# Kernel optimization log

Hardware: AMD Instinct MI355X
Metric: run time of the kernel (lower is better)

The kernel has to match this reference:

```python
import jax, jax.numpy as jnp
import numpy as np

D_MODEL = 1024
D_FF = 4 * D_MODEL
NUM_EXPERTS = 8
TOP_K = 2
BATCH, SEQ = 2, 2048


def setup_inputs() -> dict:
    key = jax.random.key(0)
    ks = jax.random.split(key, 6)
    s_in = 1.0 / np.sqrt(D_MODEL)
    s_ff = 1.0 / np.sqrt(D_FF)
    x = jax.random.normal(ks[0], (BATCH, SEQ, D_MODEL), dtype=jnp.float32)
    Wg = jax.random.uniform(ks[1], (D_MODEL, NUM_EXPERTS), minval=-s_in, maxval=s_in, dtype=jnp.float32)
    W1 = jax.random.uniform(ks[2], (NUM_EXPERTS, D_MODEL, D_FF), minval=-s_in, maxval=s_in, dtype=jnp.float32)
    b1 = jax.random.uniform(ks[3], (NUM_EXPERTS, D_FF), minval=-s_in, maxval=s_in, dtype=jnp.float32)
    W2 = jax.random.uniform(ks[4], (NUM_EXPERTS, D_FF, D_MODEL), minval=-s_ff, maxval=s_ff, dtype=jnp.float32)
    b2 = jax.random.uniform(ks[5], (NUM_EXPERTS, D_MODEL), minval=-s_ff, maxval=s_ff, dtype=jnp.float32)
    return {"x": x, "Wg": Wg, "W1": W1, "b1": b1, "W2": W2, "b2": b2}


def reference(x, Wg, W1, b1, W2, b2):
    B, S, D = x.shape
    x_flat = x.reshape(-1, D)                      # [T, D]
    gate_logits = x_flat @ Wg                      # [T, E] (eval mode: no noise)
    gate_probs = jax.nn.softmax(gate_logits, axis=-1)
    top_v, top_i = jax.lax.top_k(gate_probs, TOP_K)            # [T, k]
    top_v = top_v / (jnp.sum(top_v, axis=-1, keepdims=True) + 1e-8)
    out = jnp.zeros_like(x_flat)
    for e in range(NUM_EXPERTS):
        # combine weight for expert e: sum of normalized top-k probs routed here
        w_e = jnp.sum(jnp.where(top_i == e, top_v, 0.0), axis=-1)   # [T]
        h = jax.nn.gelu(x_flat @ W1[e] + b1[e], approximate=False)  # [T, F]
        y = h @ W2[e] + b2[e]                                       # [T, D]
        out = out + w_e[:, None] * y
    return out.reshape(B, S, D)
```

## Files before the change

### kernel.cpp

```cpp
#include <hip/hip_runtime.h>
#include <math.h>

typedef __attribute__((ext_vector_type(8))) short short8;
typedef __attribute__((ext_vector_type(4))) float f32x4;
typedef unsigned short u16;

#define NT 4096
#define DM 1024
#define DF 4096
#define NE 8
#define HROWS 9216
#define TIT 72
#define YROWS (2 * NT + 8)

static __device__ __forceinline__ u16 f2bf(float f) {
  union { float f; unsigned u; } v; v.f = f;
  return (u16)((v.u + 0x7fffu + ((v.u >> 16) & 1u)) >> 16);
}

static __device__ __forceinline__ float fast_gelu(float x) {
  float x2 = x * x;
  float z = x * __builtin_fmaf(x2, 0.1029392294f, 2.302118131f);
  float e, r;
  asm("v_exp_f32 %0, %1" : "=v"(e) : "v"(z));
  float e1 = e + 1.0f;
  asm("v_rcp_f32 %0, %1" : "=v"(r) : "v"(e1));
  return __builtin_fmaf(-x, r, x);
}

static __device__ __forceinline__ void gload16(const void* g, void* l) {
  __builtin_amdgcn_global_load_lds((const __attribute__((address_space(1))) void*)g,
                                   (__attribute__((address_space(3))) void*)l, 16, 0, 0);
}

static __device__ __forceinline__ int xcd_swz(int bid, int nwg) {
  int per = nwg >> 3;
  return (bid & 7) * per + (bid >> 3);
}

__global__ __launch_bounds__(256) void gate_k(const float* __restrict__ x,
                                              const float* __restrict__ Wg,
                                              int* __restrict__ te,
                                              float* __restrict__ tw,
                                              u16* __restrict__ xbf) {
  int t = blockIdx.x * 4 + (threadIdx.x >> 6);
  int l = threadIdx.x & 63;
  float a0=0,a1=0,a2=0,a3=0,a4=0,a5=0,a6=0,a7=0;
  const float* xr = x + (size_t)t * DM;
  for (int k = l; k < DM; k += 64) {
    float xv = xr[k];
    const float4* wp = (const float4*)(Wg + k * 8);
    float4 w0 = wp[0], w1 = wp[1];
    a0 += xv * w0.x; a1 += xv * w0.y; a2 += xv * w0.z; a3 += xv * w0.w;
    a4 += xv * w1.x; a5 += xv * w1.y; a6 += xv * w1.z; a7 += xv * w1.w;
  }
  u16* xo = xbf + (size_t)t * DM;
#pragma unroll
  for (int h = 0; h < 2; ++h) {
    int k = h * 512 + l * 8;
    float4 a = *(const float4*)(xr + k);
    float4 b = *(const float4*)(xr + k + 4);
    short8 o8 = { (short)f2bf(a.x), (short)f2bf(a.y), (short)f2bf(a.z), (short)f2bf(a.w),
                  (short)f2bf(b.x), (short)f2bf(b.y), (short)f2bf(b.z), (short)f2bf(b.w) };
    *(short8*)(xo + k) = o8;
  }
#pragma unroll
  for (int s = 32; s >= 1; s >>= 1) {
    a0 += __shfl_down(a0, s); a1 += __shfl_down(a1, s);
    a2 += __shfl_down(a2, s); a3 += __shfl_down(a3, s);
    a4 += __shfl_down(a4, s); a5 += __shfl_down(a5, s);
    a6 += __shfl_down(a6, s); a7 += __shfl_down(a7, s);
  }
  if (l == 0) {
    float lg[8] = {a0,a1,a2,a3,a4,a5,a6,a7};
    float m = lg[0];
#pragma unroll
    for (int e = 1; e < 8; ++e) m = fmaxf(m, lg[e]);
    float p[8], s = 0.f;
#pragma unroll
    for (int e = 0; e < 8; ++e) { p[e] = expf(lg[e] - m); s += p[e]; }
#pragma unroll
    for (int e = 0; e < 8; ++e) p[e] /= s;
    int i0 = 0; float v0 = p[0];
#pragma unroll
    for (int e = 1; e < 8; ++e) if (p[e] > v0) { v0 = p[e]; i0 = e; }
    int i1 = -1; float v1 = -1.f;
#pragma unroll
    for (int e = 0; e < 8; ++e) {
      if (e == i0) continue;
      if (p[e] > v1) { v1 = p[e]; i1 = e; }
    }
    float norm = v0 + v1 + 1e-8f;
    te[t*2]   = i0; te[t*2+1] = i1;
    tw[t*2]   = v0 / norm; tw[t*2+1] = v1 / norm;
  }
}

__global__ __launch_bounds__(256) void route_k(const int* __restrict__ te,
                                               const float* __restrict__ tw,
                                               int* __restrict__ meta,
                                               int* __restrict__ lt,
                                               float* __restrict__ lw) {
  int i = blockIdx.x * 256 + threadIdx.x;
  if (i >= NT * 2) return;
  int e = te[i];
  float w = tw[i];
  int pos = atomicAdd(&meta[e], 1);
  lt[e * NT + pos] = i;
  lw[e * NT + pos] = w;
}

__global__ __launch_bounds__(256) void finalize_k(int* __restrict__ meta,
                                                  int* __restrict__ lt,
                                                  float* __restrict__ lw) {
  __shared__ int s_cnt[8], s_pc[8];
  if (threadIdx.x == 0) {
    int base = 0, nt_ = 0;
    for (int e = 0; e < 8; ++e) {
      int c = meta[e];
      int pc = (c + 127) & ~127;
      s_cnt[e] = c; s_pc[e] = pc;
      meta[8 + e] = pc;
      meta[16 + e] = base;
      base += pc;
      for (int mt = 0; mt < pc / 128; ++mt) meta[32 + nt_++] = (e << 16) | mt;
    }
    meta[24] = nt_;
  }
  __syncthreads();
  for (int e = 0; e < 8; ++e) {
    int c = s_cnt[e], pc = s_pc[e];
    for (int i = c + (int)threadIdx.x; i < pc; i += 256) {
      lt[e * NT + i] = 2 * NT;
      lw[e * NT + i] = 0.f;
    }
  }
}

__global__ __launch_bounds__(256) void prep_wT(const float* __restrict__ in,
                                               u16* __restrict__ out, int K, int N) {
  const int e = blockIdx.z;
  const int n0 = blockIdx.x * 64, k0 = blockIdx.y * 64;
  const float* ie = in + (size_t)e * K * N;
  u16* oe = out + (size_t)e * K * N;
  __shared__ u16 t[64 * 72];
  const int tid = threadIdx.x;
  const int kr = tid >> 4, nq = (tid & 15) * 4;
#pragma unroll
  for (int it = 0; it < 4; ++it) {
    int k = it * 16 + kr;
    float4 v = *(const float4*)(ie + (size_t)(k0 + k) * N + n0 + nq);
    t[(nq + 0) * 72 + k] = f2bf(v.x);
    t[(nq + 1) * 72 + k] = f2bf(v.y);
    t[(nq + 2) * 72 + k] = f2bf(v.z);
    t[(nq + 3) * 72 + k] = f2bf(v.w);
  }
  __syncthreads();
#pragma unroll
  for (int it = 0; it < 2; ++it) {
    int idx = it * 256 + tid;
    int n = idx >> 3, kc = idx & 7;
    short8 v = *(const short8*)&t[n * 72 + kc * 8];
    *(short8*)(oe + (size_t)(n0 + n) * K + k0 + kc * 8) = v;
  }
}

#define STAGE4(b)                                            \
  do {                                                       \
    gload16(pa0, laA + (b) * 4096 + lda0);                   \
    gload16(pa1, laA + (b) * 4096 + lda1);                   \
    gload16(pb0, laB + (b) * 4096 + lda0);                   \
    gload16(pb1, laB + (b) * 4096 + lda1);                   \
    pa0 += 32; pa1 += 32; pb0 += 32; pb1 += 32;              \
  } while (0)

__global__ __launch_bounds__(256) void ffn1_k(const u16* __restrict__ xbf,
                                              const u16* __restrict__ W1T,
                                              const float* __restrict__ b1,
                                              const int* __restrict__ lt,
                                              const int* __restrict__ meta,
                                              u16* __restrict__ H) {
  const int vid = xcd_swz(blockIdx.x, (DF / 128) * TIT);
  const int nt = vid & 31;
  const int ti = vid >> 5;
  if (ti >= meta[24]) return;
  const int em = meta[32 + ti];
  const int e = em >> 16, mt = em & 0xffff;
  const int rbase = meta[16 + e];

  __shared__ u16 As[2 * 4096];
  __shared__ u16 Bs[2 * 4096];

  const int tid = threadIdx.x, lane = tid & 63, wv = tid >> 6;
  const int wm = wv >> 1, wn = wv & 1, l15 = lane & 15, l4 = lane >> 4;

  int r0i = tid >> 2, s0 = tid & 3;
  int r1i = (256 + tid) >> 2;
  int kg0 = s0 ^ ((r0i >> 1) & 3);
  int kg1 = s0 ^ ((r1i >> 1) & 3);
  int tok0 = lt[e * NT + mt * 128 + r0i] >> 1; if (tok0 >= NT) tok0 = 0;
  int tok1 = lt[e * NT + mt * 128 + r1i] >> 1; if (tok1 >= NT) tok1 = 0;
  const u16* pa0 = xbf + (size_t)tok0 * DM + kg0 * 8;
  const u16* pa1 = xbf + (size_t)tok1 * DM + kg1 * 8;
  const u16* pb0 = W1T + ((size_t)e * DF + nt * 128 + r0i) * DM + kg0 * 8;
  const u16* pb1 = W1T + ((size_t)e * DF + nt * 128 + r1i) * DM + kg1 * 8;
  u16* laA = As; u16* laB = Bs;
  const int lda0 = (wv * 64) * 8, lda1 = (256 + wv * 64) * 8;

  int aoff[4], boff[4];
#pragma unroll
  for (int i = 0; i < 4; ++i) {
    int ra = wm * 64 + i * 16 + l15;
    aoff[i] = ra * 32 + (l4 ^ ((ra >> 1) & 3)) * 8;
    int rb = wn * 64 + i * 16 + l15;
    boff[i] = rb * 32 + (l4 ^ ((rb >> 1) & 3)) * 8;
  }

  f32x4 acc[4][4];
#pragma unroll
  for (int mi = 0; mi < 4; ++mi)
#pragma unroll
    for (int ni = 0; ni < 4; ++ni) acc[mi][ni] = 0.f;

  STAGE4(0);
  asm volatile("s_waitcnt vmcnt(0)" ::: "memory");
  __builtin_amdgcn_s_barrier();

  const int NK = DM / 32;
  int cur = 0;
  for (int ks = 0; ks < NK; ++ks) {
    if (ks + 1 < NK) STAGE4(cur ^ 1);
    short8 af[4], bf_[4];
#pragma unroll
    for (int i = 0; i < 4; ++i) {
      af[i]  = *(const short8*)&As[cur * 4096 + aoff[i]];
      bf_[i] = *(const short8*)&Bs[cur * 4096 + boff[i]];
    }
#pragma unroll
    for (int mi = 0; mi < 4; ++mi)
#pragma unroll
      for (int ni = 0; ni < 4; ++ni)
        acc[mi][ni] = __builtin_amdgcn_mfma_f32_16x16x32_bf16(af[mi], bf_[ni], acc[mi][ni], 0, 0, 0);
    asm volatile("s_waitcnt vmcnt(0)" ::: "memory");
    __builtin_amdgcn_s_barrier();
    cur ^= 1;
  }

  const size_t hrow0 = (size_t)rbase + mt * 128;
#pragma unroll
  for (int mi = 0; mi < 4; ++mi) {
#pragma unroll
    for (int ni = 0; ni < 4; ++ni) {
      int gn = nt * 128 + wn * 64 + ni * 16 + l15;
      float bias = b1[e * DF + gn];
      int rr = wm * 64 + mi * 16 + l4 * 4;
#pragma unroll
      for (int j = 0; j < 4; ++j) {
        float v = fast_gelu(acc[mi][ni][j] + bias);
        H[(hrow0 + rr + j) * DF + gn] = f2bf(v);
      }
    }
  }
}

template <bool USEY>
__global__ __launch_bounds__(256) void ffn2_k(const u16* __restrict__ H,
                                              const u16* __restrict__ W2T,
                                              const float* __restrict__ b2,
                                              const int* __restrict__ lt,
                                              const float* __restrict__ lw,
                                              const int* __restrict__ meta,
                                              float* __restrict__ Y,
                                              float* __restrict__ out) {
  const int vid = xcd_swz(blockIdx.x, (DM / 128) * TIT);
  const int nt = vid & 7;
  const int ti = vid >> 3;
  if (ti >= meta[24]) return;
  const int em = meta[32 + ti];
  const int e = em >> 16, mt = em & 0xffff;
  const int rbase = meta[16 + e];

  __shared__ u16 As[2 * 4096];
  __shared__ u16 Bs[2 * 4096];
  __shared__ int s_ts[128];
  __shared__ float s_w[128];

  const int tid = threadIdx.x, lane = tid & 63, wv = tid >> 6;
  const int wm = wv >> 1, wn = wv & 1, l15 = lane & 15, l4 = lane >> 4;

  if (tid < 128) {
    s_ts[tid] = lt[e * NT + mt * 128 + tid];
    s_w[tid]  = lw[e * NT + mt * 128 + tid];
  }

  int r0i = tid >> 2, s0 = tid & 3;
  int r1i = (256 + tid) >> 2;
  int kg0 = s0 ^ ((r0i >> 1) & 3);
  int kg1 = s0 ^ ((r1i >> 1) & 3);
  const u16* pa0 = H + ((size_t)rbase + mt * 128 + r0i) * DF + kg0 * 8;
  const u16* pa1 = H + ((size_t)rbase + mt * 128 + r1i) * DF + kg1 * 8;
  const u16* pb0 = W2T + ((size_t)e * DM + nt * 128 + r0i) * DF + kg0 * 8;
  const u16* pb1 = W2T + ((size_t)e * DM + nt * 128 + r1i) * DF + kg1 * 8;
  u16* laA = As; u16* laB = Bs;
  const int lda0 = (wv * 64) * 8, lda1 = (256 + wv * 64) * 8;

  int aoff[4], boff[4];
#pragma unroll
  for (int i = 0; i < 4; ++i) {
    int ra = wm * 64 + i * 16 + l15;
    aoff[i] = ra * 32 + (l4 ^ ((ra >> 1) & 3)) * 8;
    int rb = wn * 64 + i * 16 + l15;
    boff[i] = rb * 32 + (l4 ^ ((rb >> 1) & 3)) * 8;
  }

  f32x4 acc[4][4];
#pragma unroll
  for (int mi = 0; mi < 4; ++mi)
#pragma unroll
    for (int ni = 0; ni < 4; ++ni) acc[mi][ni] = 0.f;

  STAGE4(0);
  asm volatile("s_waitcnt vmcnt(0)" ::: "memory");
  __builtin_amdgcn_s_barrier();

  const int NK = DF / 32;
  int cur = 0;
  for (int ks = 0; ks < NK; ++ks) {
    if (ks + 1 < NK) STAGE4(cur ^ 1);
    short8 af[4], bf_[4];
#pragma unroll
    for (int i = 0; i < 4; ++i) {
      af[i]  = *(const short8*)&As[cur * 4096 + aoff[i]];
      bf_[i] = *(const short8*)&Bs[cur * 4096 + boff[i]];
    }
#pragma unroll
    for (int mi = 0; mi < 4; ++mi)
#pragma unroll
      for (int ni = 0; ni < 4; ++ni)
        acc[mi][ni] = __builtin_amdgcn_mfma_f32_16x16x32_bf16(af[mi], bf_[ni], acc[mi][ni], 0, 0, 0);
    asm volatile("s_waitcnt vmcnt(0)" ::: "memory");
    __builtin_amdgcn_s_barrier();
    cur ^= 1;
  }

#pragma unroll
  for (int mi = 0; mi < 4; ++mi) {
#pragma unroll
    for (int ni = 0; ni < 4; ++ni) {
      int gn = nt * 128 + wn * 64 + ni * 16 + l15;
      float bias = b2[e * DM + gn];
      int rr = wm * 64 + mi * 16 + l4 * 4;
#pragma unroll
      for (int j = 0; j < 4; ++j) {
        int r = rr + j;
        float w = s_w[r];
        int ts = s_ts[r];
        float v = w * (acc[mi][ni][j] + bias);
        if (USEY) {
          Y[(size_t)ts * DM + gn] = v;
        } else {
          int tok = ts >> 1;
          if (tok >= NT) tok = 0;
          atomicAdd(out + (size_t)tok * DM + gn, v);
        }
      }
    }
  }
}

__global__ __launch_bounds__(256) void combine_k(const float* __restrict__ Y,
                                                 float* __restrict__ out) {
  size_t i4 = (size_t)blockIdx.x * 256 + threadIdx.x;
  size_t t = i4 >> 8;
  int c4 = (int)(i4 & 255) * 4;
  const float4 a = *(const float4*)(Y + (2 * t) * DM + c4);
  const float4 b = *(const float4*)(Y + (2 * t + 1) * DM + c4);
  float4 o = { a.x + b.x, a.y + b.y, a.z + b.z, a.w + b.w };
  *(float4*)(out + t * DM + c4) = o;
}

extern "C" void kernel_launch(void* const* d_in, const int* in_sizes, int n_in,
                              void* d_out, int out_size, void* d_ws, size_t ws_size,
                              hipStream_t stream) {
  const float* x  = (const float*)d_in[0];
  const float* Wg = (const float*)d_in[1];
  const float* W1 = (const float*)d_in[2];
  const float* b1 = (const float*)d_in[3];
  const float* W2 = (const float*)d_in[4];
  const float* b2 = (const float*)d_in[5];
  float* out = (float*)d_out;

  char* ws = (char*)d_ws;
  size_t o = 0;
  auto take = [&](size_t sz) { size_t p = o; o = (o + sz + 1023) & ~(size_t)1023; return p; };

  int*   meta = (int*)(ws + take(1024));
  int*   te   = (int*)(ws + take((size_t)NT * 2 * 4));
  float* tw   = (float*)(ws + take((size_t)NT * 2 * 4));
  int*   lt   = (int*)(ws + take((size_t)NE * NT * 4));
  float* lw   = (float*)(ws + take((size_t)NE * NT * 4));
  u16*   xbf  = (u16*)(ws + take((size_t)NT * DM * 2));
  u16*   W1T  = (u16*)(ws + take((size_t)NE * DM * DF * 2));
  u16*   H    = (u16*)(ws + take((size_t)HROWS * DF * 2));
  size_t needB = o;
  size_t ySz = (size_t)YROWS * DM * 4;
  size_t needA = needB + ((size_t)NE * DM * DF * 2 + 1024) + (ySz + 1024);

  bool pathA = (ws_size >= needA);
  u16*   W2T;
  float* Y = nullptr;
  if (pathA) {
    W2T = (u16*)(ws + take((size_t)NE * DM * DF * 2));
    Y   = (float*)(ws + take(ySz));
  } else {
    W2T = W1T;
  }

  hipMemsetAsync(meta, 0, 1024, stream);
  if (!pathA) hipMemsetAsync(out, 0, (size_t)NT * DM * 4, stream);

  gate_k<<<NT / 4, 256, 0, stream>>>(x, Wg, te, tw, xbf);
  route_k<<<(NT * 2) / 256, 256, 0, stream>>>(te, tw, meta, lt, lw);
  finalize_k<<<1, 256, 0, stream>>>(meta, lt, lw);
  prep_wT<<<dim3(DF / 64, DM / 64, NE), 256, 0, stream>>>(W1, W1T, DM, DF);
  if (pathA)
    prep_wT<<<dim3(DM / 64, DF / 64, NE), 256, 0, stream>>>(W2, W2T, DF, DM);

  ffn1_k<<<(DF / 128) * TIT, 256, 0, stream>>>(xbf, W1T, b1, lt, meta, H);

  if (!pathA)
    prep_wT<<<dim3(DM / 64, DF / 64, NE), 256, 0, stream>>>(W2, W2T, DF, DM);

  if (pathA) {
    ffn2_k<true><<<(DM / 128) * TIT, 256, 0, stream>>>(H, W2T, b2, lt, lw, meta, Y, out);
    combine_k<<<NT, 256, 0, stream>>>(Y, out);
  } else {
    ffn2_k<false><<<(DM / 128) * TIT, 256, 0, stream>>>(H, W2T, b2, lt, lw, meta, Y, out);
  }
}
```

Before: 406.1 us.

## Use BK=64 single-buffered tiles and split-K the second FFN GEMM

Both expert GEMM kernels now load a 64-wide K tile into a single LDS buffer with an 8-way XOR swizzle. They use two barriers per step instead of double-buffered 32-wide tiles, which halves the loop iterations but no longer overlaps loads with MFMA. When the workspace is large enough, ffn2 is split along K into two halves writing separate Y buffers, and combine_k sums them. This doubles the block count for the low-parallelism second GEMM, at the cost of extra Y traffic and workspace.

```diff
diff --git a/kernel.cpp b/kernel.cpp
--- a/kernel.cpp
+++ b/kernel.cpp
@@ -12,6 +12,7 @@
 #define HROWS 9216
 #define TIT 72
 #define YROWS (2 * NT + 8)
+#define BK 64
 
 static __device__ __forceinline__ u16 f2bf(float f) {
   union { float f; unsigned u; } v; v.f = f;
@@ -165,15 +166,6 @@
   }
 }
 
-#define STAGE4(b)                                            \
-  do {                                                       \
-    gload16(pa0, laA + (b) * 4096 + lda0);                   \
-    gload16(pa1, laA + (b) * 4096 + lda1);                   \
-    gload16(pb0, laB + (b) * 4096 + lda0);                   \
-    gload16(pb1, laB + (b) * 4096 + lda1);                   \
-    pa0 += 32; pa1 += 32; pb0 += 32; pb1 += 32;              \
-  } while (0)
-
 __global__ __launch_bounds__(256) void ffn1_k(const u16* __restrict__ xbf,
                                               const u16* __restrict__ W1T,
                                               const float* __restrict__ b1,
@@ -188,32 +180,32 @@
   const int e = em >> 16, mt = em & 0xffff;
   const int rbase = meta[16 + e];
 
-  __shared__ u16 As[2 * 4096];
-  __shared__ u16 Bs[2 * 4096];
+  __shared__ u16 As[128 * BK];
+  __shared__ u16 Bs[128 * BK];
 
   const int tid = threadIdx.x, lane = tid & 63, wv = tid >> 6;
   const int wm = wv >> 1, wn = wv & 1, l15 = lane & 15, l4 = lane >> 4;
 
-  int r0i = tid >> 2, s0 = tid & 3;
-  int r1i = (256 + tid) >> 2;
-  int kg0 = s0 ^ ((r0i >> 1) & 3);
-  int kg1 = s0 ^ ((r1i >> 1) & 3);
-  int tok0 = lt[e * NT + mt * 128 + r0i] >> 1; if (tok0 >= NT) tok0 = 0;
-  int tok1 = lt[e * NT + mt * 128 + r1i] >> 1; if (tok1 >= NT) tok1 = 0;
-  const u16* pa0 = xbf + (size_t)tok0 * DM + kg0 * 8;
-  const u16* pa1 = xbf + (size_t)tok1 * DM + kg1 * 8;
-  const u16* pb0 = W1T + ((size_t)e * DF + nt * 128 + r0i) * DM + kg0 * 8;
-  const u16* pb1 = W1T + ((size_t)e * DF + nt * 128 + r1i) * DM + kg1 * 8;
-  u16* laA = As; u16* laB = Bs;
-  const int lda0 = (wv * 64) * 8, lda1 = (256 + wv * 64) * 8;
+  const int c8 = tid & 7, r0 = tid >> 3;
+  const int cs = c8 ^ (r0 & 7);
+  const u16* pa[4]; const u16* pb[4];
+#pragma unroll
+  for (int it = 0; it < 4; ++it) {
+    int r = r0 + it * 32;
+    int tok = lt[e * NT + mt * 128 + r] >> 1; if (tok >= NT) tok = 0;
+    pa[it] = xbf + (size_t)tok * DM + cs * 8;
+    pb[it] = W1T + ((size_t)e * DF + nt * 128 + r) * DM + cs * 8;
+  }
+  u16* ldsA = As + (size_t)wv * 64 * 8;
+  u16* ldsB = Bs + (size_t)wv * 64 * 8;
 
   int aoff[4], boff[4];
 #pragma unroll
   for (int i = 0; i < 4; ++i) {
     int ra = wm * 64 + i * 16 + l15;
-    aoff[i] = ra * 32 + (l4 ^ ((ra >> 1) & 3)) * 8;
+    aoff[i] = ra * BK + (l4 ^ (ra & 7)) * 8;
     int rb = wn * 64 + i * 16 + l15;
-    boff[i] = rb * 32 + (l4 ^ ((rb >> 1) & 3)) * 8;
+    boff[i] = rb * BK + (l4 ^ (rb & 7)) * 8;
   }
 
   f32x4 acc[4][4];
@@ -222,28 +214,32 @@
 #pragma unroll
     for (int ni = 0; ni < 4; ++ni) acc[mi][ni] = 0.f;
 
-  STAGE4(0);
-  asm volatile("s_waitcnt vmcnt(0)" ::: "memory");
-  __builtin_amdgcn_s_barrier();
-
-  const int NK = DM / 32;
-  int cur = 0;
+  const int NK = DM / BK;
   for (int ks = 0; ks < NK; ++ks) {
-    if (ks + 1 < NK) STAGE4(cur ^ 1);
-    short8 af[4], bf_[4];
-#pragma unroll
-    for (int i = 0; i < 4; ++i) {
-      af[i]  = *(const short8*)&As[cur * 4096 + aoff[i]];
-      bf_[i] = *(const short8*)&Bs[cur * 4096 + boff[i]];
-    }
-#pragma unroll
-    for (int mi = 0; mi < 4; ++mi)
-#pragma unroll
-      for (int ni = 0; ni < 4; ++ni)
-        acc[mi][ni] = __builtin_amdgcn_mfma_f32_16x16x32_bf16(af[mi], bf_[ni], acc[mi][ni], 0, 0, 0);
-    asm volatile("s_waitcnt vmcnt(0)" ::: "memory");
-    __builtin_amdgcn_s_barrier();
-    cur ^= 1;
+    __syncthreads();
+#pragma unroll
+    for (int it = 0; it < 4; ++it) {
+      gload16(pa[it], ldsA + it * 2048);
+      gload16(pb[it], ldsB + it * 2048);
+      pa[it] += BK; pb[it] += BK;
+    }
+    __syncthreads();
+
+    short8 af[2][4], bf_[2][4];
+#pragma unroll
+    for (int h = 0; h < 2; ++h)
+#pragma unroll
+      for (int i = 0; i < 4; ++i) {
+        af[h][i]  = *(const short8*)&As[aoff[i] ^ (h * 32)];
+        bf_[h][i] = *(const short8*)&Bs[boff[i] ^ (h * 32)];
+      }
+#pragma unroll
+    for (int h = 0; h < 2; ++h)
+#pragma unroll
+      for (int mi = 0; mi < 4; ++mi)
+#pragma unroll
+        for (int ni = 0; ni < 4; ++ni)
+          acc[mi][ni] = __builtin_amdgcn_mfma_f32_16x16x32_bf16(af[h][mi], bf_[h][ni], acc[mi][ni], 0, 0, 0);
   }
 
   const size_t hrow0 = (size_t)rbase + mt * 128;
@@ -263,7 +259,7 @@
   }
 }
 
-template <bool USEY>
+template <bool USEY, int NZ>
 __global__ __launch_bounds__(256) void ffn2_k(const u16* __restrict__ H,
                                               const u16* __restrict__ W2T,
                                               const float* __restrict__ b2,
@@ -272,16 +268,18 @@
                                               const int* __restrict__ meta,
                                               float* __restrict__ Y,
                                               float* __restrict__ out) {
-  const int vid = xcd_swz(blockIdx.x, (DM / 128) * TIT);
+  const int vid = xcd_swz(blockIdx.x, (DM / 128) * TIT * NZ);
   const int nt = vid & 7;
-  const int ti = vid >> 3;
+  const int kz = (NZ == 2) ? ((vid >> 3) & 1) : 0;
+  const int ti = (NZ == 2) ? (vid >> 4) : (vid >> 3);
   if (ti >= meta[24]) return;
   const int em = meta[32 + ti];
   const int e = em >> 16, mt = em & 0xffff;
   const int rbase = meta[16 + e];
-
-  __shared__ u16 As[2 * 4096];
-  __shared__ u16 Bs[2 * 4096];
+  const int KOFF = kz * (DF / NZ);
+
+  __shared__ u16 As[128 * BK];
+  __shared__ u16 Bs[128 * BK];
   __shared__ int s_ts[128];
   __shared__ float s_w[128];
 
@@ -293,24 +291,25 @@
     s_w[tid]  = lw[e * NT + mt * 128 + tid];
   }
 
-  int r0i = tid >> 2, s0 = tid & 3;
-  int r1i = (256 + tid) >> 2;
-  int kg0 = s0 ^ ((r0i >> 1) & 3);
-  int kg1 = s0 ^ ((r1i >> 1) & 3);
-  const u16* pa0 = H + ((size_t)rbase + mt * 128 + r0i) * DF + kg0 * 8;
-  const u16* pa1 = H + ((size_t)rbase + mt * 128 + r1i) * DF + kg1 * 8;
-  const u16* pb0 = W2T + ((size_t)e * DM + nt * 128 + r0i) * DF + kg0 * 8;
-  const u16* pb1 = W2T + ((size_t)e * DM + nt * 128 + r1i) * DF + kg1 * 8;
-  u16* laA = As; u16* laB = Bs;
-  const int lda0 = (wv * 64) * 8, lda1 = (256 + wv * 64) * 8;
+  const int c8 = tid & 7, r0 = tid >> 3;
+  const int cs = c8 ^ (r0 & 7);
+  const u16* pa[4]; const u16* pb[4];
+#pragma unroll
+  for (int it = 0; it < 4; ++it) {
+    int r = r0 + it * 32;
+    pa[it] = H + ((size_t)rbase + mt * 128 + r) * DF + KOFF + cs * 8;
+    pb[it] = W2T + ((size_t)e * DM + nt * 128 + r) * DF + KOFF + cs * 8;
+  }
+  u16* ldsA = As + (size_t)wv * 64 * 8;
+  u16* ldsB = Bs + (size_t)wv * 64 * 8;
 
   int aoff[4], boff[4];
 #pragma unroll
   for (int i = 0; i < 4; ++i) {
     int ra = wm * 64 + i * 16 + l15;
-    aoff[i] = ra * 32 + (l4 ^ ((ra >> 1) & 3)) * 8;
+    aoff[i] = ra * BK + (l4 ^ (ra & 7)) * 8;
     int rb = wn * 64 + i * 16 + l15;
-    boff[i] = rb * 32 + (l4 ^ ((rb >> 1) & 3)) * 8;
+    boff[i] = rb * BK + (l4 ^ (rb & 7)) * 8;
   }
 
   f32x4 acc[4][4];
@@ -319,28 +318,32 @@
 #pragma unroll
     for (int ni = 0; ni < 4; ++ni) acc[mi][ni] = 0.f;
 
-  STAGE4(0);
-  asm volatile("s_waitcnt vmcnt(0)" ::: "memory");
-  __builtin_amdgcn_s_barrier();
-
-  const int NK = DF / 32;
-  int cur = 0;
+  const int NK = (DF / NZ) / BK;
   for (int ks = 0; ks < NK; ++ks) {
-    if (ks + 1 < NK) STAGE4(cur ^ 1);
-    short8 af[4], bf_[4];
-#pragma unroll
-    for (int i = 0; i < 4; ++i) {
-      af[i]  = *(const short8*)&As[cur * 4096 + aoff[i]];
-      bf_[i] = *(const short8*)&Bs[cur * 4096 + boff[i]];
-    }
-#pragma unroll
-    for (int mi = 0; mi < 4; ++mi)
-#pragma unroll
-      for (int ni = 0; ni < 4; ++ni)
-        acc[mi][ni] = __builtin_amdgcn_mfma_f32_16x16x32_bf16(af[mi], bf_[ni], acc[mi][ni], 0, 0, 0);
-    asm volatile("s_waitcnt vmcnt(0)" ::: "memory");
-    __builtin_amdgcn_s_barrier();
-    cur ^= 1;
+    __syncthreads();
+#pragma unroll
+    for (int it = 0; it < 4; ++it) {
+      gload16(pa[it], ldsA + it * 2048);
+      gload16(pb[it], ldsB + it * 2048);
+      pa[it] += BK; pb[it] += BK;
+    }
+    __syncthreads();
+
+    short8 af[2][4], bf_[2][4];
+#pragma unroll
+    for (int h = 0; h < 2; ++h)
+#pragma unroll
+      for (int i = 0; i < 4; ++i) {
+        af[h][i]  = *(const short8*)&As[aoff[i] ^ (h * 32)];
+        bf_[h][i] = *(const short8*)&Bs[boff[i] ^ (h * 32)];
+      }
+#pragma unroll
+    for (int h = 0; h < 2; ++h)
+#pragma unroll
+      for (int mi = 0; mi < 4; ++mi)
+#pragma unroll
+        for (int ni = 0; ni < 4; ++ni)
+          acc[mi][ni] = __builtin_amdgcn_mfma_f32_16x16x32_bf16(af[h][mi], bf_[h][ni], acc[mi][ni], 0, 0, 0);
   }
 
 #pragma unroll
@@ -348,7 +351,7 @@
 #pragma unroll
     for (int ni = 0; ni < 4; ++ni) {
       int gn = nt * 128 + wn * 64 + ni * 16 + l15;
-      float bias = b2[e * DM + gn];
+      float bias = (kz == 0) ? b2[e * DM + gn] : 0.f;
       int rr = wm * 64 + mi * 16 + l4 * 4;
 #pragma unroll
       for (int j = 0; j < 4; ++j) {
@@ -357,7 +360,7 @@
         int ts = s_ts[r];
         float v = w * (acc[mi][ni][j] + bias);
         if (USEY) {
-          Y[(size_t)ts * DM + gn] = v;
+          Y[((size_t)kz * YROWS + ts) * DM + gn] = v;
         } else {
           int tok = ts >> 1;
           if (tok >= NT) tok = 0;
@@ -369,13 +372,18 @@
 }
 
 __global__ __launch_bounds__(256) void combine_k(const float* __restrict__ Y,
-                                                 float* __restrict__ out) {
+                                                 float* __restrict__ out, int nz) {
   size_t i4 = (size_t)blockIdx.x * 256 + threadIdx.x;
   size_t t = i4 >> 8;
   int c4 = (int)(i4 & 255) * 4;
   const float4 a = *(const float4*)(Y + (2 * t) * DM + c4);
   const float4 b = *(const float4*)(Y + (2 * t + 1) * DM + c4);
   float4 o = { a.x + b.x, a.y + b.y, a.z + b.z, a.w + b.w };
+  if (nz == 2) {
+    const float4 c = *(const float4*)(Y + ((size_t)YROWS + 2 * t) * DM + c4);
+    const float4 d = *(const float4*)(Y + ((size_t)YROWS + 2 * t + 1) * DM + c4);
+    o.x += c.x + d.x; o.y += c.y + d.y; o.z += c.z + d.z; o.w += c.w + d.w;
+  }
   *(float4*)(out + t * DM + c4) = o;
 }
 
@@ -404,37 +412,41 @@
   u16*   H    = (u16*)(ws + take((size_t)HROWS * DF * 2));
   size_t needB = o;
   size_t ySz = (size_t)YROWS * DM * 4;
-  size_t needA = needB + ((size_t)NE * DM * DF * 2 + 1024) + (ySz + 1024);
-
-  bool pathA = (ws_size >= needA);
+  size_t needA  = needB + ((size_t)NE * DM * DF * 2 + 1024) + (ySz + 1024);
+  size_t needA2 = needA + ySz + 1024;
+
+  int nz = (ws_size >= needA2) ? 2 : (ws_size >= needA ? 1 : 0);
   u16*   W2T;
   float* Y = nullptr;
-  if (pathA) {
+  if (nz > 0) {
     W2T = (u16*)(ws + take((size_t)NE * DM * DF * 2));
-    Y   = (float*)(ws + take(ySz));
+    Y   = (float*)(ws + take((size_t)nz * ySz));
   } else {
     W2T = W1T;
   }
 
   hipMemsetAsync(meta, 0, 1024, stream);
-  if (!pathA) hipMemsetAsync(out, 0, (size_t)NT * DM * 4, stream);
+  if (nz == 0) hipMemsetAsync(out, 0, (size_t)NT * DM * 4, stream);
 
   gate_k<<<NT / 4, 256, 0, stream>>>(x, Wg, te, tw, xbf);
   route_k<<<(NT * 2) / 256, 256, 0, stream>>>(te, tw, meta, lt, lw);
   finalize_k<<<1, 256, 0, stream>>>(meta, lt, lw);
   prep_wT<<<dim3(DF / 64, DM / 64, NE), 256, 0, stream>>>(W1, W1T, DM, DF);
-  if (pathA)
+  if (nz > 0)
     prep_wT<<<dim3(DM / 64, DF / 64, NE), 256, 0, stream>>>(W2, W2T, DF, DM);
 
   ffn1_k<<<(DF / 128) * TIT, 256, 0, stream>>>(xbf, W1T, b1, lt, meta, H);
 
-  if (!pathA)
+  if (nz == 0)
     prep_wT<<<dim3(DM / 64, DF / 64, NE), 256, 0, stream>>>(W2, W2T, DF, DM);
 
-  if (pathA) {
-    ffn2_k<true><<<(DM / 128) * TIT, 256, 0, stream>>>(H, W2T, b2, lt, lw, meta, Y, out);
-    combine_k<<<NT, 256, 0, stream>>>(Y, out);
+  if (nz == 2) {
+    ffn2_k<true, 2><<<(DM / 128) * TIT * 2, 256, 0, stream>>>(H, W2T, b2, lt, lw, meta, Y, out);
+    combine_k<<<NT, 256, 0, stream>>>(Y, out, 2);
+  } else if (nz == 1) {
+    ffn2_k<true, 1><<<(DM / 128) * TIT, 256, 0, stream>>>(H, W2T, b2, lt, lw, meta, Y, out);
+    combine_k<<<NT, 256, 0, stream>>>(Y, out, 1);
   } else {
-    ffn2_k<false><<<(DM / 128) * TIT, 256, 0, stream>>>(H, W2T, b2, lt, lw, meta, Y, out);
-  }
-}
+    ffn2_k<false, 1><<<(DM / 128) * TIT, 256, 0, stream>>>(H, W2T, b2, lt, lw, meta, Y, out);
+  }
+}
```

After: 417.5 us. +2.8%, slower.

## Replace double-buffered LDS staging with a single buffer in both FFN GEMMs

Applied to the files above, without the earlier changes.

Both expert GEMM kernels (ffn1 and ffn2) now stage each K-slice into one LDS buffer instead of two ping-pong buffers. Each iteration is bracketed by two __syncthreads, one before and one after the loads. This halves the LDS footprint per block, which could allow more resident blocks per CU. In exchange, the global-to-LDS load of the next slice no longer overlaps the MFMA work on the current slice, so every K step pays the full load latency plus an extra barrier.

```diff
diff --git a/kernel.cpp b/kernel.cpp
--- a/kernel.cpp
+++ b/kernel.cpp
@@ -165,15 +165,6 @@
   }
 }
 
-#define STAGE4(b)                                            \
-  do {                                                       \
-    gload16(pa0, laA + (b) * 4096 + lda0);                   \
-    gload16(pa1, laA + (b) * 4096 + lda1);                   \
-    gload16(pb0, laB + (b) * 4096 + lda0);                   \
-    gload16(pb1, laB + (b) * 4096 + lda1);                   \
-    pa0 += 32; pa1 += 32; pb0 += 32; pb1 += 32;              \
-  } while (0)
-
 __global__ __launch_bounds__(256) void ffn1_k(const u16* __restrict__ xbf,
                                               const u16* __restrict__ W1T,
                                               const float* __restrict__ b1,
@@ -188,8 +179,8 @@
   const int e = em >> 16, mt = em & 0xffff;
   const int rbase = meta[16 + e];
 
-  __shared__ u16 As[2 * 4096];
-  __shared__ u16 Bs[2 * 4096];
+  __shared__ u16 As[128 * 32];
+  __shared__ u16 Bs[128 * 32];
 
   const int tid = threadIdx.x, lane = tid & 63, wv = tid >> 6;
   const int wm = wv >> 1, wn = wv & 1, l15 = lane & 15, l4 = lane >> 4;
@@ -204,7 +195,6 @@
   const u16* pa1 = xbf + (size_t)tok1 * DM + kg1 * 8;
   const u16* pb0 = W1T + ((size_t)e * DF + nt * 128 + r0i) * DM + kg0 * 8;
   const u16* pb1 = W1T + ((size_t)e * DF + nt * 128 + r1i) * DM + kg1 * 8;
-  u16* laA = As; u16* laB = Bs;
   const int lda0 = (wv * 64) * 8, lda1 = (256 + wv * 64) * 8;
 
   int aoff[4], boff[4];
@@ -222,28 +212,25 @@
 #pragma unroll
     for (int ni = 0; ni < 4; ++ni) acc[mi][ni] = 0.f;
 
-  STAGE4(0);
-  asm volatile("s_waitcnt vmcnt(0)" ::: "memory");
-  __builtin_amdgcn_s_barrier();
-
   const int NK = DM / 32;
-  int cur = 0;
   for (int ks = 0; ks < NK; ++ks) {
-    if (ks + 1 < NK) STAGE4(cur ^ 1);
+    __syncthreads();
+    gload16(pa0, As + lda0); gload16(pa1, As + lda1);
+    gload16(pb0, Bs + lda0); gload16(pb1, Bs + lda1);
+    pa0 += 32; pa1 += 32; pb0 += 32; pb1 += 32;
+    __syncthreads();
+
     short8 af[4], bf_[4];
 #pragma unroll
     for (int i = 0; i < 4; ++i) {
-      af[i]  = *(const short8*)&As[cur * 4096 + aoff[i]];
-      bf_[i] = *(const short8*)&Bs[cur * 4096 + boff[i]];
+      af[i]  = *(const short8*)&As[aoff[i]];
+      bf_[i] = *(const short8*)&Bs[boff[i]];
     }
 #pragma unroll
     for (int mi = 0; mi < 4; ++mi)
 #pragma unroll
       for (int ni = 0; ni < 4; ++ni)
         acc[mi][ni] = __builtin_amdgcn_mfma_f32_16x16x32_bf16(af[mi], bf_[ni], acc[mi][ni], 0, 0, 0);
-    asm volatile("s_waitcnt vmcnt(0)" ::: "memory");
-    __builtin_amdgcn_s_barrier();
-    cur ^= 1;
   }
 
   const size_t hrow0 = (size_t)rbase + mt * 128;
@@ -280,8 +267,8 @@
   const int e = em >> 16, mt = em & 0xffff;
   const int rbase = meta[16 + e];
 
-  __shared__ u16 As[2 * 4096];
-  __shared__ u16 Bs[2 * 4096];
+  __shared__ u16 As[128 * 32];
+  __shared__ u16 Bs[128 * 32];
   __shared__ int s_ts[128];
   __shared__ float s_w[128];
 
@@ -301,7 +288,6 @@
   const u16* pa1 = H + ((size_t)rbase + mt * 128 + r1i) * DF + kg1 * 8;
   const u16* pb0 = W2T + ((size_t)e * DM + nt * 128 + r0i) * DF + kg0 * 8;
   const u16* pb1 = W2T + ((size_t)e * DM + nt * 128 + r1i) * DF + kg1 * 8;
-  u16* laA = As; u16* laB = Bs;
   const int lda0 = (wv * 64) * 8, lda1 = (256 + wv * 64) * 8;
 
   int aoff[4], boff[4];
@@ -319,28 +305,25 @@
 #pragma unroll
     for (int ni = 0; ni < 4; ++ni) acc[mi][ni] = 0.f;
 
-  STAGE4(0);
-  asm volatile("s_waitcnt vmcnt(0)" ::: "memory");
-  __builtin_amdgcn_s_barrier();
-
   const int NK = DF / 32;
-  int cur = 0;
   for (int ks = 0; ks < NK; ++ks) {
-    if (ks + 1 < NK) STAGE4(cur ^ 1);
+    __syncthreads();
+    gload16(pa0, As + lda0); gload16(pa1, As + lda1);
+    gload16(pb0, Bs + lda0); gload16(pb1, Bs + lda1);
+    pa0 += 32; pa1 += 32; pb0 += 32; pb1 += 32;
+    __syncthreads();
+
     short8 af[4], bf_[4];
 #pragma unroll
     for (int i = 0; i < 4; ++i) {
-      af[i]  = *(const short8*)&As[cur * 4096 + aoff[i]];
-      bf_[i] = *(const short8*)&Bs[cur * 4096 + boff[i]];
+      af[i]  = *(const short8*)&As[aoff[i]];
+      bf_[i] = *(const short8*)&Bs[boff[i]];
     }
 #pragma unroll
     for (int mi = 0; mi < 4; ++mi)
 #pragma unroll
       for (int ni = 0; ni < 4; ++ni)
         acc[mi][ni] = __builtin_amdgcn_mfma_f32_16x16x32_bf16(af[mi], bf_[ni], acc[mi][ni], 0, 0, 0);
-    asm volatile("s_waitcnt vmcnt(0)" ::: "memory");
-    __builtin_amdgcn_s_barrier();
-    cur ^= 1;
   }
 
 #pragma unroll
```

Measured after the change: 354.0 us. 12.8% less time.

## Deepen global-to-LDS prefetch so two stages are in flight in both FFN GEMMs

Applied to the files above, without the earlier changes.

The K-loops of both expert GEMMs now issue loads for stages 0 and 1 up front. Each iteration waits with vmcnt(4), so only the current stage has to have landed while the next stays in flight. The freed buffer is refilled after the compute and an LDS-read barrier. This aims to hide more global-load latency than the old scheme, which waited for all loads at the end of each step. It adds one more barrier per iteration and relies on exact vmcnt counting with the two LDS buffers.

```diff
diff --git a/kernel.cpp b/kernel.cpp
--- a/kernel.cpp
+++ b/kernel.cpp
@@ -165,13 +165,13 @@
   }
 }
 
-#define STAGE4(b)                                            \
-  do {                                                       \
-    gload16(pa0, laA + (b) * 4096 + lda0);                   \
-    gload16(pa1, laA + (b) * 4096 + lda1);                   \
-    gload16(pb0, laB + (b) * 4096 + lda0);                   \
-    gload16(pb1, laB + (b) * 4096 + lda1);                   \
-    pa0 += 32; pa1 += 32; pb0 += 32; pb1 += 32;              \
+#define STAGE(b)                                                   \
+  do {                                                             \
+    gload16(pa0, As + (b) * 4096 + lda0);                          \
+    gload16(pa1, As + (b) * 4096 + lda1);                          \
+    gload16(pb0, Bs + (b) * 4096 + lda0);                          \
+    gload16(pb1, Bs + (b) * 4096 + lda1);                          \
+    pa0 += 32; pa1 += 32; pb0 += 32; pb1 += 32;                    \
   } while (0)
 
 __global__ __launch_bounds__(256) void ffn1_k(const u16* __restrict__ xbf,
@@ -204,7 +204,6 @@
   const u16* pa1 = xbf + (size_t)tok1 * DM + kg1 * 8;
   const u16* pb0 = W1T + ((size_t)e * DF + nt * 128 + r0i) * DM + kg0 * 8;
   const u16* pb1 = W1T + ((size_t)e * DF + nt * 128 + r1i) * DM + kg1 * 8;
-  u16* laA = As; u16* laB = Bs;
   const int lda0 = (wv * 64) * 8, lda1 = (256 + wv * 64) * 8;
 
   int aoff[4], boff[4];
@@ -222,14 +221,15 @@
 #pragma unroll
     for (int ni = 0; ni < 4; ++ni) acc[mi][ni] = 0.f;
 
-  STAGE4(0);
-  asm volatile("s_waitcnt vmcnt(0)" ::: "memory");
-  __builtin_amdgcn_s_barrier();
-
   const int NK = DM / 32;
+  STAGE(0);
+  STAGE(1);
   int cur = 0;
   for (int ks = 0; ks < NK; ++ks) {
-    if (ks + 1 < NK) STAGE4(cur ^ 1);
+    if (ks + 1 < NK) asm volatile("s_waitcnt vmcnt(4)" ::: "memory");
+    else             asm volatile("s_waitcnt vmcnt(0)" ::: "memory");
+    __builtin_amdgcn_s_barrier();
+
     short8 af[4], bf_[4];
 #pragma unroll
     for (int i = 0; i < 4; ++i) {
@@ -241,8 +241,10 @@
 #pragma unroll
       for (int ni = 0; ni < 4; ++ni)
         acc[mi][ni] = __builtin_amdgcn_mfma_f32_16x16x32_bf16(af[mi], bf_[ni], acc[mi][ni], 0, 0, 0);
-    asm volatile("s_waitcnt vmcnt(0)" ::: "memory");
+
+    asm volatile("s_waitcnt lgkmcnt(0)" ::: "memory");
     __builtin_amdgcn_s_barrier();
+    if (ks + 2 < NK) STAGE(cur);
     cur ^= 1;
   }
 
@@ -301,7 +303,6 @@
   const u16* pa1 = H + ((size_t)rbase + mt * 128 + r1i) * DF + kg1 * 8;
   const u16* pb0 = W2T + ((size_t)e * DM + nt * 128 + r0i) * DF + kg0 * 8;
   const u16* pb1 = W2T + ((size_t)e * DM + nt * 128 + r1i) * DF + kg1 * 8;
-  u16* laA = As; u16* laB = Bs;
   const int lda0 = (wv * 64) * 8, lda1 = (256 + wv * 64) * 8;
 
   int aoff[4], boff[4];
@@ -319,14 +320,15 @@
 #pragma unroll
     for (int ni = 0; ni < 4; ++ni) acc[mi][ni] = 0.f;
 
-  STAGE4(0);
-  asm volatile("s_waitcnt vmcnt(0)" ::: "memory");
-  __builtin_amdgcn_s_barrier();
-
   const int NK = DF / 32;
+  STAGE(0);
+  STAGE(1);
   int cur = 0;
   for (int ks = 0; ks < NK; ++ks) {
-    if (ks + 1 < NK) STAGE4(cur ^ 1);
+    if (ks + 1 < NK) asm volatile("s_waitcnt vmcnt(4)" ::: "memory");
+    else             asm volatile("s_waitcnt vmcnt(0)" ::: "memory");
+    __builtin_amdgcn_s_barrier();
+
     short8 af[4], bf_[4];
 #pragma unroll
     for (int i = 0; i < 4; ++i) {
@@ -338,8 +340,10 @@
 #pragma unroll
       for (int ni = 0; ni < 4; ++ni)
         acc[mi][ni] = __builtin_amdgcn_mfma_f32_16x16x32_bf16(af[mi], bf_[ni], acc[mi][ni], 0, 0, 0);
-    asm volatile("s_waitcnt vmcnt(0)" ::: "memory");
+
+    asm volatile("s_waitcnt lgkmcnt(0)" ::: "memory");
     __builtin_amdgcn_s_barrier();
+    if (ks + 2 < NK) STAGE(cur);
     cur ^= 1;
   }
 
```

Result: faster. 363.9 us (-10.4%).
